# Kernel optimization log

Measured on AMD Instinct MI355X. Metric: run time of the kernel, lower is better.

Reference implementation:

```python
import jax, jax.numpy as jnp
import numpy as np

D_MODEL = 1024
BULK_DIM = 10          # int(log2(d_model))
ADS_RADIUS = 1.0
B, N = 4, 2048


def setup_inputs() -> dict:
    key = jax.random.key(0)
    k1, k2 = jax.random.split(key, 2)
    boundary_tokens = jax.random.normal(k1, (B, N, D_MODEL), dtype=jnp.float32)
    W_b2b = jax.random.normal(k2, (D_MODEL, D_MODEL * BULK_DIM), dtype=jnp.float32) / np.sqrt(D_MODEL).astype(np.float32)
    b_b2b = jnp.zeros((D_MODEL * BULK_DIM,), dtype=jnp.float32)
    return {"boundary_tokens": boundary_tokens, "W_b2b": W_b2b, "b_b2b": b_b2b}


def _fast_marching(bulk_coords, ads_radius):
    # bulk_coords: (B, N, K, D). Sequential eikonal-style sweep through the
    # bulk depth z = 1..K; AdS warp factor L/z attenuates the front update
    # deeper into the bulk. Returns geodesics with the same shape.
    cz = jnp.moveaxis(bulk_coords, 2, 0)                 # (K, B, N, D)
    z = jnp.arange(1, bulk_coords.shape[2] + 1, dtype=bulk_coords.dtype)
    factors = ads_radius / z                             # (K,)

    def step(g, inp):
        c, f = inp
        g_new = g + f * (c - g)
        return g_new, g_new

    _, geos = jax.lax.scan(step, cz[0], (cz, factors))   # (K, B, N, D)
    return jnp.moveaxis(geos, 0, 2)                      # (B, N, K, D)


def reference(boundary_tokens, W_b2b, b_b2b):
    Bb, Nn, D = boundary_tokens.shape
    # boundary -> bulk linear projection, reshaped to (B, N, bulk_dim, D)
    bulk_coords = (boundary_tokens @ W_b2b + b_b2b).reshape(Bb, Nn, BULK_DIM, D)
    geodesics = _fast_marching(bulk_coords, ADS_RADIUS)  # (B, N, K, D)
    bulk_features = geodesics.mean(axis=2)               # (B, N, D)
    return bulk_features
```

## Files before the change

kernel.cpp:

```cpp
#include <hip/hip_runtime.h>
#include <stdint.h>


static constexpr float FW[10] = {
    0.2928968253968254f, 0.1928968253968254f, 0.1428968253968254f,
    0.1095634920634921f, 0.0845634920634921f, 0.0645634920634921f,
    0.0478968253968254f, 0.0336111111111111f, 0.0211111111111111f,
    0.0100000000000000f};

typedef __attribute__((ext_vector_type(8))) short short8;
typedef __attribute__((ext_vector_type(4))) float floatx4;
typedef __attribute__((ext_vector_type(16))) float floatx16;

__device__ inline unsigned int bf16pack2(float hi, float lo) {
    unsigned int uh = __float_as_uint(hi) + 0x8000u;
    unsigned int ul = __float_as_uint(lo) + 0x8000u;
    return __builtin_amdgcn_perm(uh, ul, 0x07060302u);
}

#define LDS_AS(p) ((__attribute__((address_space(3))) unsigned int*)(p))
#define GLB_AS(p) ((const __attribute__((address_space(1))) unsigned int*)(p))

__global__ __launch_bounds__(256) void prep(const float* __restrict__ W,
                                            const float* __restrict__ tokens,
                                            const float* __restrict__ b,
                                            unsigned short* __restrict__ Wt,
                                            float* __restrict__ beff,
                                            uint4* __restrict__ Ab,
                                            int do_cvt) {
    __shared__ float T[32 * 65];
    const int t = threadIdx.x;
    const int bid = blockIdx.x;

    if (bid < 512) {
        const int n0 = (bid & 15) * 64;
        const int k0 = (bid >> 4) * 32;
#pragma unroll
        for (int s = 0; s < 2; ++s) {
            int slot = s * 256 + t;
            int r = slot >> 4;
            int c4 = (slot & 15) * 4;
            const float4* src = (const float4*)(W + (size_t)(k0 + r) * 10240 + n0 + c4);
            float4 acc = {0.f, 0.f, 0.f, 0.f};
#pragma unroll
            for (int j = 0; j < 10; ++j) {
                float4 v = src[j * 256];
                acc.x += FW[j] * v.x; acc.y += FW[j] * v.y;
                acc.z += FW[j] * v.z; acc.w += FW[j] * v.w;
            }
            T[r * 65 + c4 + 0] = acc.x;
            T[r * 65 + c4 + 1] = acc.y;
            T[r * 65 + c4 + 2] = acc.z;
            T[r * 65 + c4 + 3] = acc.w;
        }
        __syncthreads();
#pragma unroll
        for (int s = 0; s < 2; ++s) {
            int slot = s * 256 + t;
            int nl = slot >> 3;
            int k4 = (slot & 7) * 4;
            float f0 = T[(k4 + 0) * 65 + nl];
            float f1 = T[(k4 + 1) * 65 + nl];
            float f2 = T[(k4 + 2) * 65 + nl];
            float f3 = T[(k4 + 3) * 65 + nl];
            uint2 p;
            p.x = bf16pack2(f1, f0);
            p.y = bf16pack2(f3, f2);
            *(uint2*)(Wt + (size_t)(n0 + nl) * 1024 + k0 + k4) = p;
        }
        return;
    }
    if (bid == 512) {
        const float4* src = (const float4*)b + t;
        float4 acc = {0.f, 0.f, 0.f, 0.f};
#pragma unroll
        for (int j = 0; j < 10; ++j) {
            float4 v = src[j * 256];
            acc.x += FW[j] * v.x; acc.y += FW[j] * v.y;
            acc.z += FW[j] * v.z; acc.w += FW[j] * v.w;
        }
        ((float4*)beff)[t] = acc;
        return;
    }
    if (do_cvt) {
        size_t i = (size_t)(bid - 513) * 256 + t;
        const float4* src = (const float4*)tokens + i * 2;
        float4 a0 = src[0], a1 = src[1];
        uint4 p;
        p.x = bf16pack2(a0.y, a0.x);
        p.y = bf16pack2(a0.w, a0.z);
        p.z = bf16pack2(a1.y, a1.x);
        p.w = bf16pack2(a1.w, a1.z);
        Ab[i] = p;
    }
}

__global__ __launch_bounds__(256) void gemm32(const unsigned short* __restrict__ Ab,
                                              const unsigned short* __restrict__ Wt,
                                              const float* __restrict__ beff,
                                              float* __restrict__ C) {
    __shared__ __align__(16) unsigned char As[16384];
    __shared__ __align__(16) unsigned char Bs[16384];

    const int t = threadIdx.x;
    const int lane = t & 63;
    const int w = t >> 6;
    const int l31 = lane & 31;
    const int khalf = lane >> 5;
    const int wm = (w & 1) * 64;
    const int wn = (w >> 1) * 64;
    const int bm = blockIdx.x * 128;
    const int bn = blockIdx.y * 128;

    floatx16 acc[2][2];
#pragma unroll
    for (int i = 0; i < 2; ++i)
#pragma unroll
        for (int j = 0; j < 2; ++j)
#pragma unroll
            for (int r = 0; r < 16; ++r) acc[i][j][r] = 0.f;

    const char* Abase = (const char*)Ab + (size_t)bm * 2048;
    const char* Bbase = (const char*)Wt + (size_t)bn * 2048;

    for (int k0 = 0; k0 < 1024; k0 += 64) {
#pragma unroll
        for (int i = 0; i < 4; ++i) {
            int I = w * 4 + i;
            int slot = I * 64 + lane;
            int m = slot >> 3;
            int c = (slot & 7) ^ (m & 7);
            size_t off = (size_t)m * 2048 + (size_t)k0 * 2 + c * 16;
            __builtin_amdgcn_global_load_lds(GLB_AS(Abase + off), LDS_AS(As + I * 1024), 16, 0, 0);
            __builtin_amdgcn_global_load_lds(GLB_AS(Bbase + off), LDS_AS(Bs + I * 1024), 16, 0, 0);
        }
        __syncthreads();

#pragma unroll
        for (int kk = 0; kk < 4; ++kk) {
            int c = kk * 2 + khalf;
            short8 af[2], bf[2];
#pragma unroll
            for (int tm = 0; tm < 2; ++tm) {
                int m = wm + tm * 32 + l31;
                int slot = m * 8 + (c ^ (m & 7));
                af[tm] = *(const short8*)(As + slot * 16);
            }
#pragma unroll
            for (int tn = 0; tn < 2; ++tn) {
                int n = wn + tn * 32 + l31;
                int slot = n * 8 + (c ^ (n & 7));
                bf[tn] = *(const short8*)(Bs + slot * 16);
            }
#pragma unroll
            for (int tm = 0; tm < 2; ++tm)
#pragma unroll
                for (int tn = 0; tn < 2; ++tn)
                    acc[tm][tn] = __builtin_amdgcn_mfma_f32_32x32x16_bf16(
                        af[tm], bf[tn], acc[tm][tn], 0, 0, 0);
        }
        __syncthreads();
    }

#pragma unroll
    for (int tn = 0; tn < 2; ++tn) {
        int col = bn + wn + tn * 32 + l31;
        float bias = beff[col];
#pragma unroll
        for (int tm = 0; tm < 2; ++tm) {
            int rbase = bm + wm + tm * 32 + 4 * khalf;
#pragma unroll
            for (int r = 0; r < 16; ++r) {
                int row = rbase + (r & 3) + 8 * (r >> 2);
                C[(size_t)row * 1024 + col] = acc[tm][tn][r] + bias;
            }
        }
    }
}

__global__ __launch_bounds__(256) void gemm_fb(const float* __restrict__ A,
                                               const unsigned short* __restrict__ Wt,
                                               const float* __restrict__ beff,
                                               float* __restrict__ C) {
    __shared__ __align__(16) unsigned short As[128 * 72];
    __shared__ __align__(16) unsigned char Bs[16384];

    const int t = threadIdx.x;
    const int lane = t & 63;
    const int w = t >> 6;
    const int quad = lane >> 4;
    const int l15 = lane & 15;
    const int wm = (w & 1) * 64;
    const int wn = (w >> 1) * 64;
    const int bm = blockIdx.y * 128;
    const int bn = blockIdx.x * 128;

    floatx4 acc[4][4];
#pragma unroll
    for (int i = 0; i < 4; ++i)
#pragma unroll
        for (int j = 0; j < 4; ++j) acc[i][j] = (floatx4){0.f, 0.f, 0.f, 0.f};

    const int ar = t >> 4;
    const int ac4 = (t & 15) * 4;
    const float* Abase = A + (size_t)(bm + ar) * 1024 + ac4;
    const char* WtB = (const char*)Wt;

    for (int k0 = 0; k0 < 1024; k0 += 64) {
#pragma unroll
        for (int i = 0; i < 4; ++i) {
            int I = w * 4 + i;
            int slot = I * 64 + lane;
            int nl = slot >> 3;
            int c = (slot & 7) ^ (nl & 7);
            const char* g = WtB + (size_t)(bn + nl) * 2048 + k0 * 2 + c * 16;
            __builtin_amdgcn_global_load_lds(GLB_AS(g), LDS_AS(Bs + I * 1024), 16, 0, 0);
        }
        float4 av[8];
#pragma unroll
        for (int s = 0; s < 8; ++s)
            av[s] = *(const float4*)(Abase + (size_t)(s * 16) * 1024 + k0);
#pragma unroll
        for (int s = 0; s < 8; ++s) {
            uint2 p;
            p.x = bf16pack2(av[s].y, av[s].x);
            p.y = bf16pack2(av[s].w, av[s].z);
            *(uint2*)((char*)As + (size_t)(s * 16 + ar) * 144 + ac4 * 2) = p;
        }
        __syncthreads();
#pragma unroll
        for (int kk = 0; kk < 2; ++kk) {
            short8 af[4], bf[4];
#pragma unroll
            for (int tm = 0; tm < 4; ++tm) {
                int m = wm + tm * 16 + l15;
                af[tm] = *(const short8*)((const char*)As + (size_t)m * 144 + kk * 64 + quad * 16);
            }
#pragma unroll
            for (int tn = 0; tn < 4; ++tn) {
                int n = wn + tn * 16 + l15;
                int c = kk * 4 + quad;
                int slot = n * 8 + (c ^ (n & 7));
                bf[tn] = *(const short8*)(Bs + slot * 16);
            }
#pragma unroll
            for (int tm = 0; tm < 4; ++tm)
#pragma unroll
                for (int tn = 0; tn < 4; ++tn)
                    acc[tm][tn] = __builtin_amdgcn_mfma_f32_16x16x32_bf16(
                        af[tm], bf[tn], acc[tm][tn], 0, 0, 0);
        }
        __syncthreads();
    }
#pragma unroll
    for (int tn = 0; tn < 4; ++tn) {
        int col = bn + wn + tn * 16 + l15;
        float bias = beff[col];
#pragma unroll
        for (int tm = 0; tm < 4; ++tm) {
            int row0 = bm + wm + tm * 16 + quad * 4;
#pragma unroll
            for (int r = 0; r < 4; ++r)
                C[(size_t)(row0 + r) * 1024 + col] = acc[tm][tn][r] + bias;
        }
    }
}

extern "C" void kernel_launch(void* const* d_in, const int* in_sizes, int n_in,
                              void* d_out, int out_size, void* d_ws, size_t ws_size,
                              hipStream_t stream) {
    const float* tokens = (const float*)d_in[0];
    const float* W      = (const float*)d_in[1];
    const float* b      = (const float*)d_in[2];
    float* out = (float*)d_out;

    unsigned short* Wt = (unsigned short*)d_ws;
    float* beff = (float*)((char*)d_ws + 2097152);
    unsigned short* Ab = (unsigned short*)((char*)d_ws + 2101248);

    const int big_ws = ws_size >= 2101248 + (size_t)8192 * 1024 * 2;

    if (big_ws) {
        prep<<<513 + 4096, 256, 0, stream>>>(W, tokens, b, Wt, beff, (uint4*)Ab, 1);
        gemm32<<<dim3(64, 8), 256, 0, stream>>>(Ab, Wt, beff, out);
    } else {
        prep<<<513, 256, 0, stream>>>(W, tokens, b, Wt, beff, (uint4*)Ab, 0);
        gemm_fb<<<dim3(8, 64), 256, 0, stream>>>(tokens, Wt, beff, out);
    }
}
```

Before: 131.0 us.

## Double-buffer LDS tiles in bf16 GEMM to overlap loads with MFMA

Splits the A and B shared-memory tiles into two buffers and issues the asynchronous global-to-LDS loads for the next K tile before computing the current one. The aim is to hide global load latency behind the MFMA work. It also drops the trailing barrier, leaving one sync per K step. In exchange, LDS use per block doubles to 64 KB, which may limit blocks per CU, and fully unrolling the K loop enlarges the code.

```diff
diff --git a/kernel.cpp b/kernel.cpp
--- a/kernel.cpp
+++ b/kernel.cpp
@@ -99,8 +99,8 @@
                                               const unsigned short* __restrict__ Wt,
                                               const float* __restrict__ beff,
                                               float* __restrict__ C) {
-    __shared__ __align__(16) unsigned char As[16384];
-    __shared__ __align__(16) unsigned char Bs[16384];
+    __shared__ __align__(16) unsigned char As[2][16384];
+    __shared__ __align__(16) unsigned char Bs[2][16384];
 
     const int t = threadIdx.x;
     const int lane = t & 63;
@@ -123,19 +123,40 @@
     const char* Abase = (const char*)Ab + (size_t)bm * 2048;
     const char* Bbase = (const char*)Wt + (size_t)bn * 2048;
 
-    for (int k0 = 0; k0 < 1024; k0 += 64) {
-#pragma unroll
-        for (int i = 0; i < 4; ++i) {
-            int I = w * 4 + i;
-            int slot = I * 64 + lane;
-            int m = slot >> 3;
-            int c = (slot & 7) ^ (m & 7);
-            size_t off = (size_t)m * 2048 + (size_t)k0 * 2 + c * 16;
-            __builtin_amdgcn_global_load_lds(GLB_AS(Abase + off), LDS_AS(As + I * 1024), 16, 0, 0);
-            __builtin_amdgcn_global_load_lds(GLB_AS(Bbase + off), LDS_AS(Bs + I * 1024), 16, 0, 0);
-        }
+    const int sI = w * 4;
+
+#pragma unroll
+    for (int i = 0; i < 4; ++i) {
+        int I = sI + i;
+        int slot = I * 64 + lane;
+        int m = slot >> 3;
+        int c = (slot & 7) ^ (m & 7);
+        size_t off = (size_t)m * 2048 + c * 16;
+        __builtin_amdgcn_global_load_lds(GLB_AS(Abase + off), LDS_AS(As[0] + I * 1024), 16, 0, 0);
+        __builtin_amdgcn_global_load_lds(GLB_AS(Bbase + off), LDS_AS(Bs[0] + I * 1024), 16, 0, 0);
+    }
+
+#pragma unroll
+    for (int kt = 0; kt < 16; ++kt) {
         __syncthreads();
 
+        if (kt < 15) {
+            int k0n = (kt + 1) * 64;
+            int buf = (kt + 1) & 1;
+#pragma unroll
+            for (int i = 0; i < 4; ++i) {
+                int I = sI + i;
+                int slot = I * 64 + lane;
+                int m = slot >> 3;
+                int c = (slot & 7) ^ (m & 7);
+                size_t off = (size_t)m * 2048 + (size_t)k0n * 2 + c * 16;
+                __builtin_amdgcn_global_load_lds(GLB_AS(Abase + off), LDS_AS(As[buf] + I * 1024), 16, 0, 0);
+                __builtin_amdgcn_global_load_lds(GLB_AS(Bbase + off), LDS_AS(Bs[buf] + I * 1024), 16, 0, 0);
+            }
+        }
+
+        const unsigned char* Acur = As[kt & 1];
+        const unsigned char* Bcur = Bs[kt & 1];
 #pragma unroll
         for (int kk = 0; kk < 4; ++kk) {
             int c = kk * 2 + khalf;
@@ -144,13 +165,13 @@
             for (int tm = 0; tm < 2; ++tm) {
                 int m = wm + tm * 32 + l31;
                 int slot = m * 8 + (c ^ (m & 7));
-                af[tm] = *(const short8*)(As + slot * 16);
+                af[tm] = *(const short8*)(Acur + slot * 16);
             }
 #pragma unroll
             for (int tn = 0; tn < 2; ++tn) {
                 int n = wn + tn * 32 + l31;
                 int slot = n * 8 + (c ^ (n & 7));
-                bf[tn] = *(const short8*)(Bs + slot * 16);
+                bf[tn] = *(const short8*)(Bcur + slot * 16);
             }
 #pragma unroll
             for (int tm = 0; tm < 2; ++tm)
@@ -159,7 +180,6 @@
                     acc[tm][tn] = __builtin_amdgcn_mfma_f32_32x32x16_bf16(
                         af[tm], bf[tn], acc[tm][tn], 0, 0, 0);
         }
-        __syncthreads();
     }
 
 #pragma unroll
```

After: 129.2 us. No clear change (-1.3%).

## Fuse token bf16 conversion into GEMM with double-buffered B prefetch

Applied to the files above, without the earlier changes.

The separate pass that converted the fp32 tokens to a bf16 buffer in workspace is removed. The GEMM now loads fp32 tokens into registers, packs them to bf16 and writes them into swizzled LDS itself, prefetching the next k-tile of A into registers and of B into a second LDS buffer while computing the current tile. This drops the 16 MB intermediate write and read of the converted tokens and one set of prep blocks. In exchange it adds VALU conversion work and register pressure inside the GEMM and uses more LDS per block.

```diff
diff --git a/kernel.cpp b/kernel.cpp
--- a/kernel.cpp
+++ b/kernel.cpp
@@ -9,7 +9,6 @@
     0.0100000000000000f};
 
 typedef __attribute__((ext_vector_type(8))) short short8;
-typedef __attribute__((ext_vector_type(4))) float floatx4;
 typedef __attribute__((ext_vector_type(16))) float floatx16;
 
 __device__ inline unsigned int bf16pack2(float hi, float lo) {
@@ -22,12 +21,9 @@
 #define GLB_AS(p) ((const __attribute__((address_space(1))) unsigned int*)(p))
 
 __global__ __launch_bounds__(256) void prep(const float* __restrict__ W,
-                                            const float* __restrict__ tokens,
                                             const float* __restrict__ b,
                                             unsigned short* __restrict__ Wt,
-                                            float* __restrict__ beff,
-                                            uint4* __restrict__ Ab,
-                                            int do_cvt) {
+                                            float* __restrict__ beff) {
     __shared__ float T[32 * 65];
     const int t = threadIdx.x;
     const int bid = blockIdx.x;
@@ -70,37 +66,23 @@
         }
         return;
     }
-    if (bid == 512) {
-        const float4* src = (const float4*)b + t;
-        float4 acc = {0.f, 0.f, 0.f, 0.f};
-#pragma unroll
-        for (int j = 0; j < 10; ++j) {
-            float4 v = src[j * 256];
-            acc.x += FW[j] * v.x; acc.y += FW[j] * v.y;
-            acc.z += FW[j] * v.z; acc.w += FW[j] * v.w;
-        }
-        ((float4*)beff)[t] = acc;
-        return;
-    }
-    if (do_cvt) {
-        size_t i = (size_t)(bid - 513) * 256 + t;
-        const float4* src = (const float4*)tokens + i * 2;
-        float4 a0 = src[0], a1 = src[1];
-        uint4 p;
-        p.x = bf16pack2(a0.y, a0.x);
-        p.y = bf16pack2(a0.w, a0.z);
-        p.z = bf16pack2(a1.y, a1.x);
-        p.w = bf16pack2(a1.w, a1.z);
-        Ab[i] = p;
-    }
-}
-
-__global__ __launch_bounds__(256) void gemm32(const unsigned short* __restrict__ Ab,
+    const float4* src = (const float4*)b + t;
+    float4 acc = {0.f, 0.f, 0.f, 0.f};
+#pragma unroll
+    for (int j = 0; j < 10; ++j) {
+        float4 v = src[j * 256];
+        acc.x += FW[j] * v.x; acc.y += FW[j] * v.y;
+        acc.z += FW[j] * v.z; acc.w += FW[j] * v.w;
+    }
+    ((float4*)beff)[t] = acc;
+}
+
+__global__ __launch_bounds__(256) void gemm_m(const float* __restrict__ A,
                                               const unsigned short* __restrict__ Wt,
                                               const float* __restrict__ beff,
                                               float* __restrict__ C) {
     __shared__ __align__(16) unsigned char As[16384];
-    __shared__ __align__(16) unsigned char Bs[16384];
+    __shared__ __align__(16) unsigned char Bs[2][16384];
 
     const int t = threadIdx.x;
     const int lane = t & 63;
@@ -120,22 +102,58 @@
 #pragma unroll
             for (int r = 0; r < 16; ++r) acc[i][j][r] = 0.f;
 
-    const char* Abase = (const char*)Ab + (size_t)bm * 2048;
+    const int ar = t >> 4;
+    const int ac4 = (t & 15) * 4;
+    const int c_log = ac4 >> 3;
+    const int halfo = (ac4 >> 2) & 1;
+    const float* Ap = A + (size_t)(bm + ar) * 1024 + ac4;
     const char* Bbase = (const char*)Wt + (size_t)bn * 2048;
 
-    for (int k0 = 0; k0 < 1024; k0 += 64) {
-#pragma unroll
-        for (int i = 0; i < 4; ++i) {
-            int I = w * 4 + i;
-            int slot = I * 64 + lane;
-            int m = slot >> 3;
-            int c = (slot & 7) ^ (m & 7);
-            size_t off = (size_t)m * 2048 + (size_t)k0 * 2 + c * 16;
-            __builtin_amdgcn_global_load_lds(GLB_AS(Abase + off), LDS_AS(As + I * 1024), 16, 0, 0);
-            __builtin_amdgcn_global_load_lds(GLB_AS(Bbase + off), LDS_AS(Bs + I * 1024), 16, 0, 0);
+    float4 av[8];
+#pragma unroll
+    for (int s = 0; s < 8; ++s)
+        av[s] = *(const float4*)(Ap + (size_t)(s * 16) * 1024);
+#pragma unroll
+    for (int i = 0; i < 4; ++i) {
+        int I = w * 4 + i;
+        int slot = I * 64 + lane;
+        int n = slot >> 3;
+        int c = (slot & 7) ^ (n & 7);
+        __builtin_amdgcn_global_load_lds(GLB_AS(Bbase + (size_t)n * 2048 + c * 16),
+                                         LDS_AS(Bs[0] + I * 1024), 16, 0, 0);
+    }
+
+#pragma unroll
+    for (int kt = 0; kt < 16; ++kt) {
+#pragma unroll
+        for (int s = 0; s < 8; ++s) {
+            float4 v = av[s];
+            uint2 p;
+            p.x = bf16pack2(v.y, v.x);
+            p.y = bf16pack2(v.w, v.z);
+            int m = s * 16 + ar;
+            int slot = m * 8 + (c_log ^ (m & 7));
+            *(uint2*)(As + slot * 16 + halfo * 8) = p;
         }
         __syncthreads();
 
+        if (kt < 15) {
+#pragma unroll
+            for (int s = 0; s < 8; ++s)
+                av[s] = *(const float4*)(Ap + (size_t)(s * 16) * 1024 + (kt + 1) * 64);
+#pragma unroll
+            for (int i = 0; i < 4; ++i) {
+                int I = w * 4 + i;
+                int slot = I * 64 + lane;
+                int n = slot >> 3;
+                int c = (slot & 7) ^ (n & 7);
+                __builtin_amdgcn_global_load_lds(
+                    GLB_AS(Bbase + (size_t)n * 2048 + (size_t)(kt + 1) * 128 + c * 16),
+                    LDS_AS(Bs[(kt + 1) & 1] + I * 1024), 16, 0, 0);
+            }
+        }
+
+        const unsigned char* Bcur = Bs[kt & 1];
 #pragma unroll
         for (int kk = 0; kk < 4; ++kk) {
             int c = kk * 2 + khalf;
@@ -150,7 +168,7 @@
             for (int tn = 0; tn < 2; ++tn) {
                 int n = wn + tn * 32 + l31;
                 int slot = n * 8 + (c ^ (n & 7));
-                bf[tn] = *(const short8*)(Bs + slot * 16);
+                bf[tn] = *(const short8*)(Bcur + slot * 16);
             }
 #pragma unroll
             for (int tm = 0; tm < 2; ++tm)
@@ -174,94 +192,6 @@
                 int row = rbase + (r & 3) + 8 * (r >> 2);
                 C[(size_t)row * 1024 + col] = acc[tm][tn][r] + bias;
             }
-        }
-    }
-}
-
-__global__ __launch_bounds__(256) void gemm_fb(const float* __restrict__ A,
-                                               const unsigned short* __restrict__ Wt,
-                                               const float* __restrict__ beff,
-                                               float* __restrict__ C) {
-    __shared__ __align__(16) unsigned short As[128 * 72];
-    __shared__ __align__(16) unsigned char Bs[16384];
-
-    const int t = threadIdx.x;
-    const int lane = t & 63;
-    const int w = t >> 6;
-    const int quad = lane >> 4;
-    const int l15 = lane & 15;
-    const int wm = (w & 1) * 64;
-    const int wn = (w >> 1) * 64;
-    const int bm = blockIdx.y * 128;
-    const int bn = blockIdx.x * 128;
-
-    floatx4 acc[4][4];
-#pragma unroll
-    for (int i = 0; i < 4; ++i)
-#pragma unroll
-        for (int j = 0; j < 4; ++j) acc[i][j] = (floatx4){0.f, 0.f, 0.f, 0.f};
-
-    const int ar = t >> 4;
-    const int ac4 = (t & 15) * 4;
-    const float* Abase = A + (size_t)(bm + ar) * 1024 + ac4;
-    const char* WtB = (const char*)Wt;
-
-    for (int k0 = 0; k0 < 1024; k0 += 64) {
-#pragma unroll
-        for (int i = 0; i < 4; ++i) {
-            int I = w * 4 + i;
-            int slot = I * 64 + lane;
-            int nl = slot >> 3;
-            int c = (slot & 7) ^ (nl & 7);
-            const char* g = WtB + (size_t)(bn + nl) * 2048 + k0 * 2 + c * 16;
-            __builtin_amdgcn_global_load_lds(GLB_AS(g), LDS_AS(Bs + I * 1024), 16, 0, 0);
-        }
-        float4 av[8];
-#pragma unroll
-        for (int s = 0; s < 8; ++s)
-            av[s] = *(const float4*)(Abase + (size_t)(s * 16) * 1024 + k0);
-#pragma unroll
-        for (int s = 0; s < 8; ++s) {
-            uint2 p;
-            p.x = bf16pack2(av[s].y, av[s].x);
-            p.y = bf16pack2(av[s].w, av[s].z);
-            *(uint2*)((char*)As + (size_t)(s * 16 + ar) * 144 + ac4 * 2) = p;
-        }
-        __syncthreads();
-#pragma unroll
-        for (int kk = 0; kk < 2; ++kk) {
-            short8 af[4], bf[4];
-#pragma unroll
-            for (int tm = 0; tm < 4; ++tm) {
-                int m = wm + tm * 16 + l15;
-                af[tm] = *(const short8*)((const char*)As + (size_t)m * 144 + kk * 64 + quad * 16);
-            }
-#pragma unroll
-            for (int tn = 0; tn < 4; ++tn) {
-                int n = wn + tn * 16 + l15;
-                int c = kk * 4 + quad;
-                int slot = n * 8 + (c ^ (n & 7));
-                bf[tn] = *(const short8*)(Bs + slot * 16);
-            }
-#pragma unroll
-            for (int tm = 0; tm < 4; ++tm)
-#pragma unroll
-                for (int tn = 0; tn < 4; ++tn)
-                    acc[tm][tn] = __builtin_amdgcn_mfma_f32_16x16x32_bf16(
-                        af[tm], bf[tn], acc[tm][tn], 0, 0, 0);
-        }
-        __syncthreads();
-    }
-#pragma unroll
-    for (int tn = 0; tn < 4; ++tn) {
-        int col = bn + wn + tn * 16 + l15;
-        float bias = beff[col];
-#pragma unroll
-        for (int tm = 0; tm < 4; ++tm) {
-            int row0 = bm + wm + tm * 16 + quad * 4;
-#pragma unroll
-            for (int r = 0; r < 4; ++r)
-                C[(size_t)(row0 + r) * 1024 + col] = acc[tm][tn][r] + bias;
         }
     }
 }
@@ -276,15 +206,7 @@
 
     unsigned short* Wt = (unsigned short*)d_ws;
     float* beff = (float*)((char*)d_ws + 2097152);
-    unsigned short* Ab = (unsigned short*)((char*)d_ws + 2101248);
-
-    const int big_ws = ws_size >= 2101248 + (size_t)8192 * 1024 * 2;
-
-    if (big_ws) {
-        prep<<<513 + 4096, 256, 0, stream>>>(W, tokens, b, Wt, beff, (uint4*)Ab, 1);
-        gemm32<<<dim3(64, 8), 256, 0, stream>>>(Ab, Wt, beff, out);
-    } else {
-        prep<<<513, 256, 0, stream>>>(W, tokens, b, Wt, beff, (uint4*)Ab, 0);
-        gemm_fb<<<dim3(8, 64), 256, 0, stream>>>(tokens, Wt, beff, out);
-    }
-}
+
+    prep<<<513, 256, 0, stream>>>(W, b, Wt, beff);
+    gemm_m<<<dim3(64, 8), 256, 0, stream>>>(tokens, Wt, beff, out);
+}
```

Result: slower. 140.7 us (+7.4%).
